# Kernel tuning notes

Hardware: AMD Instinct MI355X
Metric: run time of the kernel (lower is better)

Reference implementation:

```python
import jax, jax.numpy as jnp
import numpy as np

STRIDES = (8, 16, 32, 64, 128)
THRESHOLD = 0.5
B, C = 8, 80
HS = (160, 80, 40, 20, 10)


def setup_inputs() -> dict:
    key = jax.random.key(0)
    ks = jax.random.split(key, 3 * len(HS))
    d = {}
    for i, h in enumerate(HS):
        d[f"cls_{i}"] = jax.random.normal(ks[3 * i], (B, C, h, h), jnp.float32)
        d[f"bbox_{i}"] = jax.random.normal(ks[3 * i + 1], (B, 4, h, h), jnp.float32)
        d[f"ctr_{i}"] = jax.random.normal(ks[3 * i + 2], (B, 1, h, h), jnp.float32)
    return d


def _filter_level(cls, bbox, ctr, stride, thr):
    # cls: [B,C,H,W], bbox: [B,4,H,W], ctr: [B,1,H,W] (NCHW, as asserted in source)
    b, c, h, w = cls.shape
    scores = cls.transpose(0, 2, 3, 1).reshape(b, h * w, c)   # [B,HW,C]
    bboxes = bbox.transpose(0, 2, 3, 1).reshape(b, h * w, 4)  # [B,HW,4]
    ctrs = ctr.transpose(0, 2, 3, 1).reshape(b, h * w, 1)     # [B,HW,1]
    # FilterModule keeps locations whose max class score exceeds threshold.
    mask = (jnp.max(scores, axis=-1) > thr)[..., None].astype(scores.dtype)  # [B,HW,1]
    ys, xs = jnp.meshgrid(jnp.arange(h), jnp.arange(w), indexing="ij")
    half = stride // 2
    coord = jnp.stack([xs * stride + half, ys * stride + half], axis=-1)  # [H,W,2]
    coord = coord.reshape(h * w, 2).astype(scores.dtype)
    coord = jnp.broadcast_to(coord, (b, h * w, 2))
    # Static-shape compaction: zero out non-selected locations instead of
    # producing dynamic-length per-image lists (jit-compatible equivalent of
    # the per-image coord/score/bbox/centerness gather).
    return jnp.concatenate(
        [coord * mask, scores * mask, bboxes * mask, ctrs * mask], axis=-1
    )  # [B, HW, 2 + C + 4 + 1]


def reference(cls_0, bbox_0, ctr_0, cls_1, bbox_1, ctr_1, cls_2, bbox_2, ctr_2,
              cls_3, bbox_3, ctr_3, cls_4, bbox_4, ctr_4):
    levels = [
        (cls_0, bbox_0, ctr_0),
        (cls_1, bbox_1, ctr_1),
        (cls_2, bbox_2, ctr_2),
        (cls_3, bbox_3, ctr_3),
        (cls_4, bbox_4, ctr_4),
    ]
    return tuple(
        _filter_level(c, bb, ct, s, THRESHOLD)
        for (c, bb, ct), s in zip(levels, STRIDES)
    )
```

## Files before the change

### kernel.cpp

```cpp
#include <hip/hip_runtime.h>

#define TILE  64
#define LS    67
#define OUTCH 87
#define NF4   1392

typedef float f32x4 __attribute__((ext_vector_type(4)));

__global__ __launch_bounds__(256) void fcos_filter_kernel(
    const float* __restrict__ cl0, const float* __restrict__ bb0, const float* __restrict__ ct0,
    const float* __restrict__ cl1, const float* __restrict__ bb1, const float* __restrict__ ct1,
    const float* __restrict__ cl2, const float* __restrict__ bb2, const float* __restrict__ ct2,
    const float* __restrict__ cl3, const float* __restrict__ bb3, const float* __restrict__ ct3,
    const float* __restrict__ cl4, const float* __restrict__ bb4, const float* __restrict__ ct4,
    float* __restrict__ out)
{
    __shared__ float lds[85 * LS];
    __shared__ float s_flag[TILE];

    const int P   = blockIdx.x;
    const int tid = threadIdx.x;

    const float *cls, *bbx, *ctr;
    int HW, W, str, ksh, iA, tA, iB, tB;
    size_t obase;
    if (P < 1600)      { cls=cl0;bbx=bb0;ctr=ct0;HW=25600;W=160;str=8;  ksh=4;obase=0u;
        const int a=2*P;        iA=a/400; tA=a-iA*400; const int b=a+1; iB=b/400; tB=b-iB*400; }
    else if (P < 2000) { cls=cl1;bbx=bb1;ctr=ct1;HW=6400; W=80; str=16; ksh=3;obase=17817600u;
        const int a=2*(P-1600); iA=a/100; tA=a-iA*100; const int b=a+1; iB=b/100; tB=b-iB*100; }
    else if (P < 2100) { cls=cl2;bbx=bb2;ctr=ct2;HW=1600; W=40; str=32; ksh=2;obase=22272000u;
        const int a=2*(P-2000); iA=a/25;  tA=a-iA*25;  const int b=a+1; iB=b/25;  tB=b-iB*25;  }
    else if (P < 2128) { cls=cl3;bbx=bb3;ctr=ct3;HW=400;  W=20; str=64; ksh=1;obase=23385600u;
        const int a=2*(P-2100); iA=a/7;   tA=a-iA*7;   const int b=a+1; iB=b/7;   tB=b-iB*7;   }
    else               { cls=cl4;bbx=bb4;ctr=ct4;HW=100;  W=10; str=128;ksh=0;obase=23664000u;
        const int a=2*(P-2128); iA=a>>1;  tA=a&1;      const int b=a+1; iB=b>>1;  tB=b&1;      }

    const int pA = tA * TILE, pB = tB * TILE;
    const int vA = min(TILE, HW - pA), vB = min(TILE, HW - pB);

    const int  lane_c = tid >> 4;
    const int  q4     = (tid & 15) << 2;
    const bool okA    = q4 < vA, okB = q4 < vB;

    auto load_tile = [&](float4 v[6], int img_, int p0_, bool ok_) {
        if (ok_) {
            const float* ab = cls + ((size_t)img_ * 80 + lane_c) * HW + p0_ + q4;
            v[0] = *reinterpret_cast<const float4*>(ab);
            v[1] = *reinterpret_cast<const float4*>(ab + (size_t)16 * HW);
            v[2] = *reinterpret_cast<const float4*>(ab + (size_t)32 * HW);
            v[3] = *reinterpret_cast<const float4*>(ab + (size_t)48 * HW);
            v[4] = *reinterpret_cast<const float4*>(ab + (size_t)64 * HW);
            if (tid < 80) {
                const float* s5 = (lane_c < 4)
                    ? bbx + ((size_t)img_ * 4 + lane_c) * HW + p0_ + q4
                    : ctr + (size_t)img_ * HW + p0_ + q4;
                v[5] = *reinterpret_cast<const float4*>(s5);
            }
        }
    };

    auto commit_tile = [&](const float4 v[6], bool ok_) {
        float4 fm; fm.x = fm.y = fm.z = fm.w = -1e30f;
        if (ok_) {
            #pragma unroll
            for (int k = 0; k < 5; ++k) {
                const int a_ = (16 * k + lane_c) * LS + q4;
                lds[a_ + 0] = v[k].x; lds[a_ + 1] = v[k].y;
                lds[a_ + 2] = v[k].z; lds[a_ + 3] = v[k].w;
                fm.x = fmaxf(fm.x, v[k].x);
                fm.y = fmaxf(fm.y, v[k].y);
                fm.z = fmaxf(fm.z, v[k].z);
                fm.w = fmaxf(fm.w, v[k].w);
            }
            if (tid < 80) {
                const int a_ = (80 + lane_c) * LS + q4;
                lds[a_ + 0] = v[5].x; lds[a_ + 1] = v[5].y;
                lds[a_ + 2] = v[5].z; lds[a_ + 3] = v[5].w;
            }
        }
        fm.x = fmaxf(fm.x, __shfl_xor(fm.x, 16));
        fm.y = fmaxf(fm.y, __shfl_xor(fm.y, 16));
        fm.z = fmaxf(fm.z, __shfl_xor(fm.z, 16));
        fm.w = fmaxf(fm.w, __shfl_xor(fm.w, 16));
        fm.x = fmaxf(fm.x, __shfl_xor(fm.x, 32));
        fm.y = fmaxf(fm.y, __shfl_xor(fm.y, 32));
        fm.z = fmaxf(fm.z, __shfl_xor(fm.z, 32));
        fm.w = fmaxf(fm.w, __shfl_xor(fm.w, 32));
        if (tid < TILE) s_flag[tid] = 0.0f;
        __syncthreads();
        if ((tid & 63) < 16) {
            if (fm.x > 0.5f) s_flag[q4 + 0] = 1.0f;
            if (fm.y > 0.5f) s_flag[q4 + 1] = 1.0f;
            if (fm.z > 0.5f) s_flag[q4 + 2] = 1.0f;
            if (fm.w > 0.5f) s_flag[q4 + 3] = 1.0f;
        }
        __syncthreads();
    };

    auto store_tile = [&](int img_, int p0_, int valid_) {
        float* dst = out + obase + ((size_t)img_ * HW + p0_) * OUTCH;
        const int nmax = valid_ * OUTCH;
        #pragma unroll
        for (int r = 0; r < 6; ++r) {
            const int f4 = tid + 256 * r;
            if (r == 5 && f4 >= NF4) break;
            const int e0 = f4 * 4;
            if (e0 >= nmax) break;
            const int p  = e0 / OUTCH;
            const int ch = e0 - p * OUTCH;
            float vals[4];
            #pragma unroll
            for (int j = 0; j < 4; ++j) {
                int chj = ch + j, pj = p;
                if (chj >= OUTCH) { chj -= OUTCH; pj += 1; }
                const float m = s_flag[pj];
                float val;
                if (chj >= 2) {
                    val = lds[(chj - 2) * LS + pj] * m;
                } else {
                    const int pg = p0_ + pj;
                    const int tt = pg >> ksh;
                    const int y  = tt / 10;
                    const int x  = pg - y * W;
                    val = (float)(((chj == 0) ? x : y) * str + (str >> 1)) * m;
                }
                vals[j] = val;
            }
            if (e0 + 4 <= nmax) {
                f32x4 o; o.x = vals[0]; o.y = vals[1]; o.z = vals[2]; o.w = vals[3];
                *reinterpret_cast<f32x4*>(dst + e0) = o;
            } else {
                #pragma unroll
                for (int j = 0; j < 4; ++j)
                    if (e0 + j < nmax) dst[e0 + j] = vals[j];
            }
        }
    };

    float4 va[6], vb[6];
    load_tile(va, iA, pA, okA);
    commit_tile(va, okA);
    load_tile(vb, iB, pB, okB);
    store_tile(iA, pA, vA);
    __syncthreads();
    commit_tile(vb, okB);
    store_tile(iB, pB, vB);
}

extern "C" void kernel_launch(void* const* d_in, const int* in_sizes, int n_in,
                              void* d_out, int out_size, void* d_ws, size_t ws_size,
                              hipStream_t stream) {
    (void)in_sizes; (void)n_in; (void)out_size; (void)d_ws; (void)ws_size;
    fcos_filter_kernel<<<2136, 256, 0, stream>>>(
        (const float*)d_in[0],  (const float*)d_in[1],  (const float*)d_in[2],
        (const float*)d_in[3],  (const float*)d_in[4],  (const float*)d_in[5],
        (const float*)d_in[6],  (const float*)d_in[7],  (const float*)d_in[8],
        (const float*)d_in[9],  (const float*)d_in[10], (const float*)d_in[11],
        (const float*)d_in[12], (const float*)d_in[13], (const float*)d_in[14],
        (float*)d_out);
}
```

Baseline: 36.45 us.

## Use one 128-position tile per 512-thread block instead of two pipelined 64-tiles

Replaces the per-block two-tile software pipeline (load B while storing A) with a single 128-position tile handled by 512 threads. Each wave loads 16 positions across all channel rows, so the class-max reduction stays inside the wave via shuffles. This removes the flag-clear syncs, leaving one barrier per block. The cost is losing the load/store overlap within a block and using twice the LDS per block, which lowers occupancy.

```diff
diff --git a/kernel.cpp b/kernel.cpp
--- a/kernel.cpp
+++ b/kernel.cpp
@@ -1,13 +1,12 @@
 #include <hip/hip_runtime.h>
 
-#define TILE  64
-#define LS    67
+#define TILE  128
+#define LS    131
 #define OUTCH 87
-#define NF4   1392
 
 typedef float f32x4 __attribute__((ext_vector_type(4)));
 
-__global__ __launch_bounds__(256) void fcos_filter_kernel(
+__global__ __launch_bounds__(512) void fcos_filter_kernel(
     const float* __restrict__ cl0, const float* __restrict__ bb0, const float* __restrict__ ct0,
     const float* __restrict__ cl1, const float* __restrict__ bb1, const float* __restrict__ ct1,
     const float* __restrict__ cl2, const float* __restrict__ bb2, const float* __restrict__ ct2,
@@ -18,140 +17,132 @@
     __shared__ float lds[85 * LS];
     __shared__ float s_flag[TILE];
 
-    const int P   = blockIdx.x;
+    const int bid = blockIdx.x;
     const int tid = threadIdx.x;
 
     const float *cls, *bbx, *ctr;
-    int HW, W, str, ksh, iA, tA, iB, tB;
+    int img, tile, HW, W, str, ksh;
     size_t obase;
-    if (P < 1600)      { cls=cl0;bbx=bb0;ctr=ct0;HW=25600;W=160;str=8;  ksh=4;obase=0u;
-        const int a=2*P;        iA=a/400; tA=a-iA*400; const int b=a+1; iB=b/400; tB=b-iB*400; }
-    else if (P < 2000) { cls=cl1;bbx=bb1;ctr=ct1;HW=6400; W=80; str=16; ksh=3;obase=17817600u;
-        const int a=2*(P-1600); iA=a/100; tA=a-iA*100; const int b=a+1; iB=b/100; tB=b-iB*100; }
-    else if (P < 2100) { cls=cl2;bbx=bb2;ctr=ct2;HW=1600; W=40; str=32; ksh=2;obase=22272000u;
-        const int a=2*(P-2000); iA=a/25;  tA=a-iA*25;  const int b=a+1; iB=b/25;  tB=b-iB*25;  }
-    else if (P < 2128) { cls=cl3;bbx=bb3;ctr=ct3;HW=400;  W=20; str=64; ksh=1;obase=23385600u;
-        const int a=2*(P-2100); iA=a/7;   tA=a-iA*7;   const int b=a+1; iB=b/7;   tB=b-iB*7;   }
-    else               { cls=cl4;bbx=bb4;ctr=ct4;HW=100;  W=10; str=128;ksh=0;obase=23664000u;
-        const int a=2*(P-2128); iA=a>>1;  tA=a&1;      const int b=a+1; iB=b>>1;  tB=b&1;      }
+    if (bid < 1600)      { cls=cl0;bbx=bb0;ctr=ct0;HW=25600;W=160;str=8;  ksh=4;obase=0u;
+                           img = bid / 200;            tile = bid - img * 200; }
+    else if (bid < 2000) { cls=cl1;bbx=bb1;ctr=ct1;HW=6400; W=80; str=16; ksh=3;obase=17817600u;
+                           const int b = bid - 1600;   img = b / 50;  tile = b - img * 50; }
+    else if (bid < 2104) { cls=cl2;bbx=bb2;ctr=ct2;HW=1600; W=40; str=32; ksh=2;obase=22272000u;
+                           const int b = bid - 2000;   img = b / 13;  tile = b - img * 13; }
+    else if (bid < 2136) { cls=cl3;bbx=bb3;ctr=ct3;HW=400;  W=20; str=64; ksh=1;obase=23385600u;
+                           const int b = bid - 2104;   img = b >> 2;  tile = b & 3; }
+    else                 { cls=cl4;bbx=bb4;ctr=ct4;HW=100;  W=10; str=128;ksh=0;obase=23664000u;
+                           img = bid - 2136;           tile = 0; }
 
-    const int pA = tA * TILE, pB = tB * TILE;
-    const int vA = min(TILE, HW - pA), vB = min(TILE, HW - pB);
+    const int p0    = tile * TILE;
+    const int valid = min(TILE, HW - p0);
 
-    const int  lane_c = tid >> 4;
-    const int  q4     = (tid & 15) << 2;
-    const bool okA    = q4 < vA, okB = q4 < vB;
+    const int w    = tid >> 6;
+    const int lane = tid & 63;
+    const int r16  = lane >> 2;
+    const int q4   = (lane & 3) << 2;
+    const int pos  = 16 * w + q4;
+    const bool ok  = pos < valid;
 
-    auto load_tile = [&](float4 v[6], int img_, int p0_, bool ok_) {
-        if (ok_) {
-            const float* ab = cls + ((size_t)img_ * 80 + lane_c) * HW + p0_ + q4;
-            v[0] = *reinterpret_cast<const float4*>(ab);
-            v[1] = *reinterpret_cast<const float4*>(ab + (size_t)16 * HW);
-            v[2] = *reinterpret_cast<const float4*>(ab + (size_t)32 * HW);
-            v[3] = *reinterpret_cast<const float4*>(ab + (size_t)48 * HW);
-            v[4] = *reinterpret_cast<const float4*>(ab + (size_t)64 * HW);
-            if (tid < 80) {
-                const float* s5 = (lane_c < 4)
-                    ? bbx + ((size_t)img_ * 4 + lane_c) * HW + p0_ + q4
-                    : ctr + (size_t)img_ * HW + p0_ + q4;
-                v[5] = *reinterpret_cast<const float4*>(s5);
+    float4 v[5];
+    float4 fm; fm.x = fm.y = fm.z = fm.w = -1e30f;
+    if (ok) {
+        const float* ab = cls + ((size_t)img * 80 + r16) * HW + p0 + pos;
+        #pragma unroll
+        for (int k = 0; k < 5; ++k) {
+            v[k] = *reinterpret_cast<const float4*>(ab + (size_t)(16 * k) * HW);
+            fm.x = fmaxf(fm.x, v[k].x);
+            fm.y = fmaxf(fm.y, v[k].y);
+            fm.z = fmaxf(fm.z, v[k].z);
+            fm.w = fmaxf(fm.w, v[k].w);
+        }
+    }
+    float4 v5;
+    const int c5   = tid >> 5;
+    const int pos5 = (tid & 31) << 2;
+    const bool ok5 = (tid < 160) && (pos5 < valid);
+    if (ok5) {
+        const float* s5 = (c5 < 4)
+            ? bbx + ((size_t)img * 4 + c5) * HW + p0 + pos5
+            : ctr + (size_t)img * HW + p0 + pos5;
+        v5 = *reinterpret_cast<const float4*>(s5);
+    }
+
+    if (ok) {
+        #pragma unroll
+        for (int k = 0; k < 5; ++k) {
+            const int a = (16 * k + r16) * LS + pos;
+            lds[a + 0] = v[k].x; lds[a + 1] = v[k].y;
+            lds[a + 2] = v[k].z; lds[a + 3] = v[k].w;
+        }
+    }
+    if (ok5) {
+        const int a = (80 + c5) * LS + pos5;
+        lds[a + 0] = v5.x; lds[a + 1] = v5.y;
+        lds[a + 2] = v5.z; lds[a + 3] = v5.w;
+    }
+
+    #pragma unroll
+    for (int m = 4; m <= 32; m <<= 1) {
+        fm.x = fmaxf(fm.x, __shfl_xor(fm.x, m));
+        fm.y = fmaxf(fm.y, __shfl_xor(fm.y, m));
+        fm.z = fmaxf(fm.z, __shfl_xor(fm.z, m));
+        fm.w = fmaxf(fm.w, __shfl_xor(fm.w, m));
+    }
+    if (lane < 4) {
+        const int fp = 16 * w + 4 * lane;
+        s_flag[fp + 0] = (fm.x > 0.5f) ? 1.0f : 0.0f;
+        s_flag[fp + 1] = (fm.y > 0.5f) ? 1.0f : 0.0f;
+        s_flag[fp + 2] = (fm.z > 0.5f) ? 1.0f : 0.0f;
+        s_flag[fp + 3] = (fm.w > 0.5f) ? 1.0f : 0.0f;
+    }
+
+    __syncthreads();
+
+    float* dst = out + obase + ((size_t)img * HW + p0) * OUTCH;
+    const int nmax = valid * OUTCH;
+    #pragma unroll
+    for (int r = 0; r < 6; ++r) {
+        const int f4 = tid + 512 * r;
+        if (r == 5 && f4 >= (TILE * OUTCH) / 4) break;
+        const int e0 = f4 * 4;
+        if (e0 >= nmax) break;
+        const int p  = e0 / OUTCH;
+        const int ch = e0 - p * OUTCH;
+        float vals[4];
+        #pragma unroll
+        for (int j = 0; j < 4; ++j) {
+            int chj = ch + j, pj = p;
+            if (chj >= OUTCH) { chj -= OUTCH; pj += 1; }
+            const float m = s_flag[pj];
+            float val;
+            if (chj >= 2) {
+                val = lds[(chj - 2) * LS + pj] * m;
+            } else {
+                const int pg = p0 + pj;
+                const int tt = pg >> ksh;
+                const int y  = tt / 10;
+                const int x  = pg - y * W;
+                val = (float)(((chj == 0) ? x : y) * str + (str >> 1)) * m;
             }
+            vals[j] = val;
         }
-    };
-
-    auto commit_tile = [&](const float4 v[6], bool ok_) {
-        float4 fm; fm.x = fm.y = fm.z = fm.w = -1e30f;
-        if (ok_) {
+        if (e0 + 4 <= nmax) {
+            f32x4 o; o.x = vals[0]; o.y = vals[1]; o.z = vals[2]; o.w = vals[3];
+            *reinterpret_cast<f32x4*>(dst + e0) = o;
+        } else {
             #pragma unroll
-            for (int k = 0; k < 5; ++k) {
-                const int a_ = (16 * k + lane_c) * LS + q4;
-                lds[a_ + 0] = v[k].x; lds[a_ + 1] = v[k].y;
-                lds[a_ + 2] = v[k].z; lds[a_ + 3] = v[k].w;
-                fm.x = fmaxf(fm.x, v[k].x);
-                fm.y = fmaxf(fm.y, v[k].y);
-                fm.z = fmaxf(fm.z, v[k].z);
-                fm.w = fmaxf(fm.w, v[k].w);
-            }
-            if (tid < 80) {
-                const int a_ = (80 + lane_c) * LS + q4;
-                lds[a_ + 0] = v[5].x; lds[a_ + 1] = v[5].y;
-                lds[a_ + 2] = v[5].z; lds[a_ + 3] = v[5].w;
-            }
+            for (int j = 0; j < 4; ++j)
+                if (e0 + j < nmax) dst[e0 + j] = vals[j];
         }
-        fm.x = fmaxf(fm.x, __shfl_xor(fm.x, 16));
-        fm.y = fmaxf(fm.y, __shfl_xor(fm.y, 16));
-        fm.z = fmaxf(fm.z, __shfl_xor(fm.z, 16));
-        fm.w = fmaxf(fm.w, __shfl_xor(fm.w, 16));
-        fm.x = fmaxf(fm.x, __shfl_xor(fm.x, 32));
-        fm.y = fmaxf(fm.y, __shfl_xor(fm.y, 32));
-        fm.z = fmaxf(fm.z, __shfl_xor(fm.z, 32));
-        fm.w = fmaxf(fm.w, __shfl_xor(fm.w, 32));
-        if (tid < TILE) s_flag[tid] = 0.0f;
-        __syncthreads();
-        if ((tid & 63) < 16) {
-            if (fm.x > 0.5f) s_flag[q4 + 0] = 1.0f;
-            if (fm.y > 0.5f) s_flag[q4 + 1] = 1.0f;
-            if (fm.z > 0.5f) s_flag[q4 + 2] = 1.0f;
-            if (fm.w > 0.5f) s_flag[q4 + 3] = 1.0f;
-        }
-        __syncthreads();
-    };
-
-    auto store_tile = [&](int img_, int p0_, int valid_) {
-        float* dst = out + obase + ((size_t)img_ * HW + p0_) * OUTCH;
-        const int nmax = valid_ * OUTCH;
-        #pragma unroll
-        for (int r = 0; r < 6; ++r) {
-            const int f4 = tid + 256 * r;
-            if (r == 5 && f4 >= NF4) break;
-            const int e0 = f4 * 4;
-            if (e0 >= nmax) break;
-            const int p  = e0 / OUTCH;
-            const int ch = e0 - p * OUTCH;
-            float vals[4];
-            #pragma unroll
-            for (int j = 0; j < 4; ++j) {
-                int chj = ch + j, pj = p;
-                if (chj >= OUTCH) { chj -= OUTCH; pj += 1; }
-                const float m = s_flag[pj];
-                float val;
-                if (chj >= 2) {
-                    val = lds[(chj - 2) * LS + pj] * m;
-                } else {
-                    const int pg = p0_ + pj;
-                    const int tt = pg >> ksh;
-                    const int y  = tt / 10;
-                    const int x  = pg - y * W;
-                    val = (float)(((chj == 0) ? x : y) * str + (str >> 1)) * m;
-                }
-                vals[j] = val;
-            }
-            if (e0 + 4 <= nmax) {
-                f32x4 o; o.x = vals[0]; o.y = vals[1]; o.z = vals[2]; o.w = vals[3];
-                *reinterpret_cast<f32x4*>(dst + e0) = o;
-            } else {
-                #pragma unroll
-                for (int j = 0; j < 4; ++j)
-                    if (e0 + j < nmax) dst[e0 + j] = vals[j];
-            }
-        }
-    };
-
-    float4 va[6], vb[6];
-    load_tile(va, iA, pA, okA);
-    commit_tile(va, okA);
-    load_tile(vb, iB, pB, okB);
-    store_tile(iA, pA, vA);
-    __syncthreads();
-    commit_tile(vb, okB);
-    store_tile(iB, pB, vB);
+    }
 }
 
 extern "C" void kernel_launch(void* const* d_in, const int* in_sizes, int n_in,
                               void* d_out, int out_size, void* d_ws, size_t ws_size,
                               hipStream_t stream) {
     (void)in_sizes; (void)n_in; (void)out_size; (void)d_ws; (void)ws_size;
-    fcos_filter_kernel<<<2136, 256, 0, stream>>>(
+    fcos_filter_kernel<<<2144, 512, 0, stream>>>(
         (const float*)d_in[0],  (const float*)d_in[1],  (const float*)d_in[2],
         (const float*)d_in[3],  (const float*)d_in[4],  (const float*)d_in[5],
         (const float*)d_in[6],  (const float*)d_in[7],  (const float*)d_in[8],
```

After: 37.12 us. About the same (+1.8%).
